# Kernel optimization log

Hardware: AMD Instinct MI355X
Metric: run time of the kernel (lower is better)

## Reference

```python
import jax, jax.numpy as jnp
import numpy as np

B, N, D = 4, 2048, 1024
H, A, Lv = 8, 128, 128   # heads, attention_dim (qk), linear_dim (v)
NUM_BLOCKS = 4
QKV_W = (2 * Lv + 2 * A) * H  # 4096
NEG = -1e9


def setup_inputs() -> dict:
    key = jax.random.key(0)
    ks = jax.random.split(key, 10)
    past_lengths = jax.random.randint(ks[0], (B,), 0, N)
    past_ids = jax.random.randint(ks[1], (B, N), 0, 10000)
    past_embeddings = jax.random.normal(ks[2], (B, N, D), dtype=jnp.float32)
    # per-block parameters, stacked on leading block axis (xavier-ish scale)
    qkv_w = jax.random.normal(ks[3], (NUM_BLOCKS, D, QKV_W), dtype=jnp.float32) * (1.0 / np.sqrt(D))
    qkv_b = jnp.zeros((NUM_BLOCKS, QKV_W), dtype=jnp.float32)
    out_w = jax.random.normal(ks[4], (NUM_BLOCKS, Lv * H, D), dtype=jnp.float32) * (1.0 / np.sqrt(Lv * H))
    out_b = jnp.zeros((NUM_BLOCKS, D), dtype=jnp.float32)
    ln_g = jnp.ones((NUM_BLOCKS, D), dtype=jnp.float32)
    ln_b = jnp.zeros((NUM_BLOCKS, D), dtype=jnp.float32)
    return {"past_lengths": past_lengths, "past_ids": past_ids,
            "past_embeddings": past_embeddings, "qkv_w": qkv_w, "qkv_b": qkv_b,
            "out_w": out_w, "out_b": out_b, "ln_g": ln_g, "ln_b": ln_b}


def _layer_norm(x, g, b, eps=1e-5):
    mu = jnp.mean(x, axis=-1, keepdims=True)
    var = jnp.mean(jnp.square(x - mu), axis=-1, keepdims=True)
    return (x - mu) * jax.lax.rsqrt(var + eps) * g + b


def _block(x, mask, qw, qb, ow, ob, g, b):
    xn = _layer_norm(x, g, b)
    qkv = (xn @ qw + qb).reshape(B, N, H, 2 * Lv + 2 * A)
    q = qkv[..., :A]              # [B,N,H,A]
    k = qkv[..., A:2 * A]         # [B,N,H,A]
    v = qkv[..., 2 * A:2 * A + Lv]  # [B,N,H,Lv]
    scores = jnp.einsum('bnha,bmha->bhnm', q, k) / np.sqrt(A)
    # original: masked_fill(-inf) -> silu -> /N -> softmax; we mask after the
    # silu transform with a large-negative logit so masked weights are ~0
    logits = jnp.where(mask[:, None, :, :], jax.nn.silu(scores) / N, NEG)
    w = jax.nn.softmax(logits, axis=-1)
    attn = jnp.einsum('bhnm,bmhl->bnhl', w, v).reshape(B, N, H * Lv)
    return x + attn @ ow + ob


def reference(past_lengths, past_ids, past_embeddings, qkv_w, qkv_b, out_w, out_b, ln_g, ln_b):
    valid = past_ids != 0                                   # [B,N]
    causal = jnp.triu(jnp.ones((N, N), dtype=bool), k=1)     # faithful to buffer (triu, diag=1)
    mask = causal[None] & valid[:, None, :] & valid[:, :, None]  # [B,N,N]
    x = past_embeddings
    for i in range(NUM_BLOCKS):
        x = _block(x, mask, qkv_w[i], qkv_b[i], out_w[i], out_b[i], ln_g[i], ln_b[i])
    return x
```

## Files before the change

kernel.cpp:

```cpp
#include <hip/hip_runtime.h>

typedef __bf16 bf16_t;
typedef __bf16 bf16x8 __attribute__((ext_vector_type(8)));
typedef __bf16 bf16x4 __attribute__((ext_vector_type(4)));
typedef float f32x4 __attribute__((ext_vector_type(4)));
typedef unsigned int u32x4 __attribute__((ext_vector_type(4)));

#define B_ 4
#define N_ 2048
#define D_ 1024
#define H_ 8
#define NB_ 4
#define M_ (B_*N_)
#define QN_ 3072
#define QKN_ 2048

__device__ __forceinline__ void async_copy16(const void* gsrc, void* ldst) {
    __builtin_amdgcn_global_load_lds(
        (const __attribute__((address_space(1))) void*)gsrc,
        (__attribute__((address_space(3))) void*)ldst, 16, 0, 0);
}

static constexpr size_t WT_OFF  = 0;
static constexpr size_t WT_SZ   = (size_t)NB_*QN_*D_*2;
static constexpr size_t OWT_OFF = WT_OFF + WT_SZ;
static constexpr size_t OWT_SZ  = (size_t)NB_*D_*D_*2;
static constexpr size_t XN_OFF  = OWT_OFF + OWT_SZ;
static constexpr size_t XN_SZ   = (size_t)M_*D_*2;
static constexpr size_t QK_OFF  = XN_OFF + XN_SZ;
static constexpr size_t QK_SZ   = (size_t)M_*QKN_*2;
static constexpr size_t VT_OFF  = QK_OFF + QK_SZ;
static constexpr size_t VT_SZ   = (size_t)32*128*N_*2;
static constexpr size_t ATT_OFF = VT_OFF + VT_SZ;
static constexpr size_t ATT_SZ  = (size_t)M_*D_*2;
static constexpr size_t QBR_OFF = ATT_OFF + ATT_SZ;
static constexpr size_t QBR_SZ  = (size_t)NB_*QN_*4;
static constexpr size_t VS_OFF  = QBR_OFF + QBR_SZ;
static constexpr size_t VS_SZ   = (size_t)NB_*32*128*4;
static constexpr size_t MASK_OFF = VS_OFF + VS_SZ;

__global__ __launch_bounds__(256) void repack_qkvw(const float* __restrict__ qw, bf16_t* __restrict__ wt)
{
    __shared__ float tile[64][65];
    const int nb = blockIdx.z;
    const int j0 = blockIdx.x * 64, d0 = blockIdx.y * 64;
    const int tx = threadIdx.x, ty = threadIdx.y;
    const float* src = qw + (size_t)nb * D_ * 4096;
    const int jj = j0 + tx;
    const int sel = jj >> 10, rr = jj & 1023, hh = rr >> 7, aa = rr & 127;
    const int orig = hh * 512 + sel * 128 + aa;
#pragma unroll
    for (int it = 0; it < 16; ++it) {
        int dr = it * 4 + ty;
        tile[dr][tx] = src[(size_t)(d0 + dr) * 4096 + orig];
    }
    __syncthreads();
    bf16_t* dst = wt + (size_t)nb * QN_ * D_;
#pragma unroll
    for (int it = 0; it < 16; ++it) {
        int jr = it * 4 + ty;
        dst[(size_t)(j0 + jr) * D_ + d0 + tx] = (bf16_t)tile[tx][jr];
    }
}

__global__ __launch_bounds__(256) void repack_outw(const float* __restrict__ ow, bf16_t* __restrict__ owt)
{
    __shared__ float tile[64][65];
    const int nb = blockIdx.z;
    const int j0 = blockIdx.x * 64, d0 = blockIdx.y * 64;
    const int tx = threadIdx.x, ty = threadIdx.y;
    const float* src = ow + (size_t)nb * D_ * D_;
#pragma unroll
    for (int it = 0; it < 16; ++it) {
        int dr = it * 4 + ty;
        tile[dr][tx] = src[(size_t)(d0 + dr) * D_ + j0 + tx];
    }
    __syncthreads();
    bf16_t* dst = owt + (size_t)nb * D_ * D_;
#pragma unroll
    for (int it = 0; it < 16; ++it) {
        int jr = it * 4 + ty;
        dst[(size_t)(j0 + jr) * D_ + d0 + tx] = (bf16_t)tile[tx][jr];
    }
}

__global__ __launch_bounds__(256) void repack_qb(const float* __restrict__ qb, float* __restrict__ qbr)
{
    int idx = blockIdx.x * 256 + threadIdx.x;
    int nb = idx / QN_, jj = idx % QN_;
    int sel = jj >> 10, rr = jj & 1023, hh = rr >> 7, aa = rr & 127;
    qbr[idx] = qb[nb * 4096 + hh * 512 + sel * 128 + aa];
}

__global__ __launch_bounds__(256) void mask_kernel(const int* __restrict__ past_ids, unsigned short* __restrict__ maskA,
                                                   float* __restrict__ vsl)
{
    const int idx = blockIdx.x * 256 + threadIdx.x;
    vsl[idx] = 0.f; vsl[idx + 8192] = 0.f;
    const int b = idx >> 11, P = idx & 2047;
    const int k = P & 31;
    const int m = (P & ~31) | (((k >> 2) & 1) << 4) | (((k >> 3) & 3) << 2) | (k & 3);
    maskA[idx] = past_ids[b * N_ + m] != 0 ? 0xFFFFu : 0u;
}

__global__ __launch_bounds__(256) void ln_kernel(const float* __restrict__ x, const float* __restrict__ g,
                                                 const float* __restrict__ bb, bf16_t* __restrict__ xn)
{
    const int row = blockIdx.x, tid = threadIdx.x;
    const float4 v = ((const float4*)(x + (size_t)row * D_))[tid];
    float s = v.x + v.y + v.z + v.w;
    float q = v.x * v.x + v.y * v.y + v.z * v.z + v.w * v.w;
#pragma unroll
    for (int d = 32; d >= 1; d >>= 1) { s += __shfl_xor(s, d); q += __shfl_xor(q, d); }
    __shared__ float ls[4], lq[4];
    if ((tid & 63) == 0) { ls[tid >> 6] = s; lq[tid >> 6] = q; }
    __syncthreads();
    s = ls[0] + ls[1] + ls[2] + ls[3];
    q = lq[0] + lq[1] + lq[2] + lq[3];
    const float mean = s * (1.f / 1024.f);
    const float var  = q * (1.f / 1024.f) - mean * mean;
    const float inv  = rsqrtf(var + 1e-5f);
    const float4 gg = ((const float4*)g)[tid];
    const float4 bv = ((const float4*)bb)[tid];
    bf16x4 o;
    o[0] = (bf16_t)((v.x - mean) * inv * gg.x + bv.x);
    o[1] = (bf16_t)((v.y - mean) * inv * gg.y + bv.y);
    o[2] = (bf16_t)((v.z - mean) * inv * gg.z + bv.z);
    o[3] = (bf16_t)((v.w - mean) * inv * gg.w + bv.w);
    *(bf16x4*)(xn + (size_t)row * D_ + tid * 4) = o;
}

__global__ __launch_bounds__(512, 2) void gemm_qkv(const bf16_t* __restrict__ Am, const bf16_t* __restrict__ Bt,
                                                   const float* __restrict__ bias,
                                                   bf16_t* __restrict__ outQK, bf16_t* __restrict__ vtOut,
                                                   float* __restrict__ vsOut)
{
    __shared__ bf16_t As[2 * 16384];
    __shared__ bf16_t Bs[2 * 12288];
    const int tid = threadIdx.x;
    const int lane = tid & 63, wave = tid >> 6;
    const int wr = wave >> 2, wc = wave & 3;
    const int quad = lane >> 4, l15 = lane & 15;
    const int swz = quad ^ ((l15 >> 1) & 3);
    const int slane8 = ((lane & 3) ^ ((lane >> 3) & 3)) * 8;
    const int lrow = lane >> 2;
    const int m0 = blockIdx.y * 256, n0 = blockIdx.x * 192;
    const int Kn = D_;

    const bf16_t* gA[4]; bf16_t* dA[4];
    const bf16_t* gB[3]; bf16_t* dB[3];
#pragma unroll
    for (int u = 0; u < 4; ++u) {
        const int a = wave * 4 + u, ch = a >> 1, hf = a & 1;
        gA[u] = Am + (size_t)(m0 + ch * 16 + lrow) * Kn + hf * 32 + slane8;
        dA[u] = &As[hf * 8192 + ch * 512 + lane * 8];
    }
#pragma unroll
    for (int u = 0; u < 3; ++u) {
        const int b = wave * 3 + u, ch = b >> 1, hf = b & 1;
        gB[u] = Bt + (size_t)(n0 + ch * 16 + lrow) * Kn + hf * 32 + slane8;
        dB[u] = &Bs[hf * 6144 + ch * 512 + lane * 8];
    }

    auto STAGE = [&](int slot) {
#pragma unroll
        for (int u = 0; u < 4; ++u) { async_copy16(gA[u], dA[u] + slot * 16384); gA[u] += 64; }
#pragma unroll
        for (int u = 0; u < 3; ++u) { async_copy16(gB[u], dB[u] + slot * 12288); gB[u] += 64; }
    };

    f32x4 acc[8][3] = {};
    const int NT = Kn >> 6;

    STAGE(0);
    asm volatile("s_waitcnt vmcnt(0)" ::: "memory");
    __builtin_amdgcn_s_barrier();

    const int abase = wr * 4096 + l15 * 32 + swz * 8;
    const int bbase = wc * 1536 + l15 * 32 + swz * 8;

    for (int t = 0; t < NT; ++t) {
        const int slot = t & 1;
        const bf16_t* ra = &As[slot * 16384 + abase];
        const bf16_t* rb = &Bs[slot * 12288 + bbase];
        if (t + 1 < NT) STAGE(slot ^ 1);
        __builtin_amdgcn_s_setprio(1);
#pragma unroll
        for (int hf = 0; hf < 2; ++hf) {
            bf16x8 af[8], bfv[3];
#pragma unroll
            for (int j = 0; j < 3; ++j) bfv[j] = *(const bf16x8*)(rb + hf * 6144 + j * 512);
#pragma unroll
            for (int i = 0; i < 8; ++i) af[i] = *(const bf16x8*)(ra + hf * 8192 + i * 512);
#pragma unroll
            for (int i = 0; i < 8; ++i)
#pragma unroll
                for (int j = 0; j < 3; ++j)
                    acc[i][j] = __builtin_amdgcn_mfma_f32_16x16x32_bf16(af[i], bfv[j], acc[i][j], 0, 0, 0);
        }
        __builtin_amdgcn_s_setprio(0);
        if (t + 1 < NT) asm volatile("s_waitcnt vmcnt(0)" ::: "memory");
        __builtin_amdgcn_s_barrier();
    }

    const int bb2 = m0 >> 11;
    int colgj[3]; float bvj[3];
#pragma unroll
    for (int j = 0; j < 3; ++j) { colgj[j] = n0 + wc * 48 + j * 16 + l15; bvj[j] = bias[colgj[j]]; }
    float ps[3] = {0.f, 0.f, 0.f};
#pragma unroll
    for (int i = 0; i < 8; ++i) {
        const int rowg = m0 + wr * 128 + i * 16 + quad * 4;
        const int mloc = rowg & 2047;
        const int mperm = (mloc & ~31) | (((mloc >> 2) & 3) << 3) | (((mloc >> 4) & 1) << 2);
#pragma unroll
        for (int j = 0; j < 3; ++j) {
            const int colg = colgj[j];
            const float bv = bvj[j];
            if (colg >= 2048) {
                const int hh = (colg - 2048) >> 7, ll = (colg - 2048) & 127;
                bf16x4 sv;
#pragma unroll
                for (int r = 0; r < 4; ++r) { sv[r] = (bf16_t)(acc[i][j][r] + bv); ps[j] += acc[i][j][r]; }
                *(bf16x4*)(vtOut + ((size_t)(bb2 * 8 + hh) * 128 + ll) * (size_t)N_ + mperm) = sv;
            } else {
                const float qs = (colg < 1024) ? 0.08838834764831845f : 1.f;
#pragma unroll
                for (int r = 0; r < 4; ++r)
                    outQK[(size_t)(rowg + r) * QKN_ + colg] = (bf16_t)((acc[i][j][r] + bv) * qs);
            }
        }
    }
#pragma unroll
    for (int j = 0; j < 3; ++j) {
        const int colg = colgj[j];
        if (colg >= 2048) {
            const int hh = (colg - 2048) >> 7, ll = (colg - 2048) & 127;
            float p = ps[j] + 32.f * bvj[j];
            p += __shfl_xor(p, 16);
            p += __shfl_xor(p, 32);
            if (quad == 0) atomicAdd(&vsOut[(size_t)(bb2 * 8 + hh) * 128 + ll], p);
        }
    }
}

__global__ __launch_bounds__(512, 2) void gemm_out(const bf16_t* __restrict__ Am, const bf16_t* __restrict__ Bt,
                                                   const float* __restrict__ bias,
                                                   const float* __restrict__ resid_in, float* __restrict__ resid_out)
{
    __shared__ bf16_t As[4 * 256 * 32];
    __shared__ bf16_t Bs[4 * 128 * 32];
    const int tid = threadIdx.x;
    const int lane = tid & 63, wave = tid >> 6;
    const int wr = wave >> 2, wc = wave & 3;
    const int quad = lane >> 4, l15 = lane & 15;
    const int swz = quad ^ ((l15 >> 1) & 3);
    const int slane8 = ((lane & 3) ^ ((lane >> 3) & 3)) * 8;
    const int lrow = lane >> 2;
    const int m0 = blockIdx.y * 256, n0 = blockIdx.x * 128;
    const int Kn = D_;

    const int chA0 = wave * 2, chA1 = chA0 + 1;
    const bf16_t* gA0 = Am + (size_t)(m0 + chA0 * 16 + lrow) * Kn + slane8;
    const bf16_t* gA1 = Am + (size_t)(m0 + chA1 * 16 + lrow) * Kn + slane8;
    const bf16_t* gB  = Bt + (size_t)(n0 + wave * 16 + lrow) * Kn + slane8;
    bf16_t* const dA0 = &As[chA0 * 512 + lane * 8];
    bf16_t* const dA1 = &As[chA1 * 512 + lane * 8];
    bf16_t* const dB  = &Bs[wave * 512 + lane * 8];

    auto STAGE = [&](int slot) {
        async_copy16(gA0, dA0 + slot * 8192);
        async_copy16(gA1, dA1 + slot * 8192);
        async_copy16(gB,  dB  + slot * 4096);
        gA0 += 32; gA1 += 32; gB += 32;
    };

    f32x4 acc[8][2] = {};
    const int NT = Kn >> 5;

    STAGE(0); STAGE(1); STAGE(2);
    asm volatile("s_waitcnt vmcnt(6)" ::: "memory");
    __builtin_amdgcn_s_barrier();

    const int aoff = (wr * 128 + l15) * 32 + swz * 8;
    const int boff = (wc * 32  + l15) * 32 + swz * 8;

    for (int t = 0; t < NT; ++t) {
        const int ring = t & 3;
        const bf16_t* ra = &As[ring * 8192 + aoff];
        const bf16_t* rb = &Bs[ring * 4096 + boff];
        bf16x8 af[8], bfv[2];
#pragma unroll
        for (int j = 0; j < 2; ++j) bfv[j] = *(const bf16x8*)(rb + j * 512);
#pragma unroll
        for (int i = 0; i < 8; ++i) af[i] = *(const bf16x8*)(ra + i * 512);
        if (t + 3 < NT) STAGE((t + 3) & 3);
        __builtin_amdgcn_s_setprio(1);
#pragma unroll
        for (int i = 0; i < 8; ++i)
#pragma unroll
            for (int j = 0; j < 2; ++j)
                acc[i][j] = __builtin_amdgcn_mfma_f32_16x16x32_bf16(af[i], bfv[j], acc[i][j], 0, 0, 0);
        __builtin_amdgcn_s_setprio(0);
        if (t + 3 < NT)      asm volatile("s_waitcnt vmcnt(6)" ::: "memory");
        else if (t + 2 < NT) asm volatile("s_waitcnt vmcnt(3)" ::: "memory");
        else if (t + 1 < NT) asm volatile("s_waitcnt vmcnt(0)" ::: "memory");
        __builtin_amdgcn_s_barrier();
    }

#pragma unroll
    for (int i = 0; i < 8; ++i) {
#pragma unroll
        for (int j = 0; j < 2; ++j) {
            const int colg = n0 + wc * 32 + j * 16 + l15;
            const float bv = bias[colg];
#pragma unroll
            for (int r = 0; r < 4; ++r) {
                const int rowg = m0 + wr * 128 + i * 16 + quad * 4 + r;
                const size_t off = (size_t)rowg * D_ + colg;
                resid_out[off] = resid_in[off] + acc[i][j][r] + bv;
            }
        }
    }
}

template<bool CAUSAL>
__device__ __forceinline__ void attn_tile(
    int m0, int m0n, int n0, int b, int h,
    const bf16_t* __restrict__ qk, const bf16_t* __restrict__ vtb,
    const unsigned short* __restrict__ maskB,
    bf16_t* Ks, bf16_t* Vs,
    const bf16x8 (&qf)[2][4], bf16x8 onesf,
    f32x4 (&oacc)[2][8], f32x4 (&dacc)[2])
{
    const int tid = threadIdx.x, lane = tid & 63, wave = tid >> 6;
    const int quad = lane >> 4, l15 = lane & 15;
    const int swz = quad ^ ((l15 >> 1) & 3);
    const int slane8 = ((lane & 3) ^ ((lane >> 3) & 3)) * 8;
    const int lrow = lane >> 2;
    const float invN = 1.f / 2048.f;

#pragma unroll
    for (int s = 0; s < 8; ++s) {
        const int kkc = s & 3, rg = (s >> 2) + wave * 2;
        async_copy16(vtb + (size_t)(rg * 16 + lrow) * N_ + m0 + kkc * 32 + slane8,
                     &Vs[kkc * 4096 + rg * 512 + lane * 8]);
    }
    bf16x8 mAf[4];
#pragma unroll
    for (int kk = 0; kk < 4; ++kk)
        mAf[kk] = *(const bf16x8*)(maskB + m0 + kk * 32 + quad * 8);

    f32x4 sacc[2][8] = {};
    __builtin_amdgcn_s_setprio(1);
#pragma unroll
    for (int kk = 0; kk < 4; ++kk) {
#pragma unroll
        for (int j = 0; j < 8; ++j) {
            bf16x8 kf = *(const bf16x8*)&Ks[kk * 4096 + (j * 16 + l15) * 32 + swz * 8];
            sacc[0][j] = __builtin_amdgcn_mfma_f32_16x16x32_bf16(kf, qf[0][kk], sacc[0][j], 0, 0, 0);
            sacc[1][j] = __builtin_amdgcn_mfma_f32_16x16x32_bf16(kf, qf[1][kk], sacc[1][j], 0, 0, 0);
        }
    }
    __builtin_amdgcn_s_setprio(0);

    bf16x8 pf[2][4];
#pragma unroll
    for (int kk = 0; kk < 4; ++kk) {
#pragma unroll
        for (int s = 0; s < 2; ++s) {
            const int j = kk * 2 + s;
#pragma unroll
            for (int nb = 0; nb < 2; ++nb) {
#pragma unroll
                for (int r = 0; r < 4; ++r) {
                    const float sv = sacc[nb][j][r];
                    const float xc = __builtin_amdgcn_fmed3f(sv, -4.f, 4.f);
                    float sg = __builtin_fmaf(xc, 0.25f * invN, 0.5f * invN);
                    sg = __builtin_fmaf(-(xc * (0.03125f * invN)), fabsf(xc), sg);
                    float e = __builtin_fmaf(sv, sg, 1.f);
                    if (CAUSAL) {
                        const int dmn = (m0 + j * 16 + quad * 4 + r) - (n0 + wave * 32 + nb * 16 + l15);
                        e = (dmn > 0) ? e : 0.f;
                    }
                    pf[nb][kk][s * 4 + r] = (bf16_t)e;
                }
            }
        }
        *(u32x4*)&pf[0][kk] = *(u32x4*)&pf[0][kk] & *(const u32x4*)&mAf[kk];
        *(u32x4*)&pf[1][kk] = *(u32x4*)&pf[1][kk] & *(const u32x4*)&mAf[kk];
    }

    __syncthreads();

    if (m0n < N_) {
        const size_t baseq = (size_t)b * N_ * QKN_;
#pragma unroll
        for (int s = 0; s < 8; ++s) {
            const int kkc = s & 3, rg = (s >> 2) + wave * 2;
            async_copy16(qk + baseq + (size_t)(m0n + rg * 16 + lrow) * QKN_ + 1024 + h * 128 + kkc * 32 + slane8,
                         &Ks[kkc * 4096 + rg * 512 + lane * 8]);
        }
    }

    __builtin_amdgcn_s_setprio(1);
#pragma unroll
    for (int kk = 0; kk < 4; ++kk) {
        dacc[0] = __builtin_amdgcn_mfma_f32_16x16x32_bf16(pf[0][kk], onesf, dacc[0], 0, 0, 0);
        dacc[1] = __builtin_amdgcn_mfma_f32_16x16x32_bf16(pf[1][kk], onesf, dacc[1], 0, 0, 0);
#pragma unroll
        for (int j = 0; j < 8; ++j) {
            bf16x8 vf = *(const bf16x8*)&Vs[kk * 4096 + (j * 16 + l15) * 32 + swz * 8];
            oacc[0][j] = __builtin_amdgcn_mfma_f32_16x16x32_bf16(pf[0][kk], vf, oacc[0][j], 0, 0, 0);
            oacc[1][j] = __builtin_amdgcn_mfma_f32_16x16x32_bf16(pf[1][kk], vf, oacc[1][j], 0, 0, 0);
        }
    }
    __builtin_amdgcn_s_setprio(0);
    __syncthreads();
}

__global__ __launch_bounds__(256, 2) void attn_kernel(const bf16_t* __restrict__ qk, const bf16_t* __restrict__ vt,
                                                      const int* __restrict__ past_ids, const float* __restrict__ vsum,
                                                      const unsigned short* __restrict__ maskA,
                                                      bf16_t* __restrict__ att)
{
    __shared__ bf16_t Ks[4 * 128 * 32];
    __shared__ bf16_t Vs[4 * 128 * 32];

    const int bx = blockIdx.x;
    const int bh = bx & 31, g = bx >> 5;
    const int t = (g < 8) ? g : 23 - g;
    const int b = bh >> 3, h = bh & 7;
    const int n0 = t << 7;
    const int tid = threadIdx.x, lane = tid & 63, wave = tid >> 6;
    const int quad = lane >> 4, l15 = lane & 15;
    const int slane8 = ((lane & 3) ^ ((lane >> 3) & 3)) * 8;
    const int lrow = lane >> 2;
    const bf16_t* vtb = vt + (size_t)bh * 128 * N_;
    const unsigned short* maskB = maskA + b * N_;
    const float invN = 1.f / 2048.f;

    bf16x8 qf[2][4];
#pragma unroll
    for (int nb = 0; nb < 2; ++nb) {
        const bf16_t* gq = qk + (size_t)b * N_ * QKN_ + (size_t)(n0 + wave * 32 + nb * 16 + l15) * QKN_ + h * 128 + quad * 8;
#pragma unroll
        for (int kk = 0; kk < 4; ++kk) qf[nb][kk] = *(const bf16x8*)(gq + kk * 32);
    }
    const float vnf0 = past_ids[b * N_ + n0 + wave * 32 + l15] != 0 ? 1.f : 0.f;
    const float vnf1 = past_ids[b * N_ + n0 + wave * 32 + 16 + l15] != 0 ? 1.f : 0.f;
    bf16x8 onesf;
#pragma unroll
    for (int i = 0; i < 8; ++i) onesf[i] = (bf16_t)1.f;

    {
        const size_t baseq = (size_t)b * N_ * QKN_;
#pragma unroll
        for (int s = 0; s < 8; ++s) {
            const int kkc = s & 3, rg = (s >> 2) + wave * 2;
            async_copy16(qk + baseq + (size_t)(n0 + rg * 16 + lrow) * QKN_ + 1024 + h * 128 + kkc * 32 + slane8,
                         &Ks[kkc * 4096 + rg * 512 + lane * 8]);
        }
    }
    __syncthreads();

    f32x4 oacc[2][8] = {};
    f32x4 dacc[2] = {};

    attn_tile<true>(n0, n0 + 128, n0, b, h, qk, vtb, maskB, Ks, Vs, qf, onesf, oacc, dacc);
    for (int m0 = n0 + 128; m0 < N_; m0 += 128)
        attn_tile<false>(m0, m0 + 128, n0, b, h, qk, vtb, maskB, Ks, Vs, qf, onesf, oacc, dacc);

    float vsr[8];
#pragma unroll
    for (int j = 0; j < 8; ++j) vsr[j] = vsum[bh * 128 + j * 16 + l15];
#pragma unroll
    for (int nb = 0; nb < 2; ++nb) {
        const float vn = nb ? vnf1 : vnf0;
#pragma unroll
        for (int r = 0; r < 4; ++r) {
            const float dn = dacc[nb][r];
            const bool uni = (vn == 0.f) || !(dn > 0.f);
            const float rc = uni ? 0.f : __builtin_amdgcn_rcpf(dn);
            const int gn = n0 + wave * 32 + nb * 16 + quad * 4 + r;
#pragma unroll
            for (int j = 0; j < 8; ++j) {
                const float ov = uni ? (vsr[j] * invN) : (oacc[nb][j][r] * rc);
                att[(size_t)(b * N_ + gn) * 1024 + h * 128 + j * 16 + l15] = (bf16_t)ov;
            }
        }
    }
}

extern "C" void kernel_launch(void* const* d_in, const int* in_sizes, int n_in,
                              void* d_out, int out_size, void* d_ws, size_t ws_size,
                              hipStream_t stream) {
    (void)in_sizes; (void)n_in; (void)out_size; (void)ws_size;
    const int*   past_ids = (const int*)d_in[1];
    const float* past_emb = (const float*)d_in[2];
    const float* qkv_w    = (const float*)d_in[3];
    const float* qkv_b    = (const float*)d_in[4];
    const float* out_w    = (const float*)d_in[5];
    const float* out_b    = (const float*)d_in[6];
    const float* ln_g     = (const float*)d_in[7];
    const float* ln_b     = (const float*)d_in[8];

    float* x = (float*)d_out;
    char* ws = (char*)d_ws;
    bf16_t* WT  = (bf16_t*)(ws + WT_OFF);
    bf16_t* OWT = (bf16_t*)(ws + OWT_OFF);
    bf16_t* XN  = (bf16_t*)(ws + XN_OFF);
    bf16_t* QK  = (bf16_t*)(ws + QK_OFF);
    bf16_t* VT  = (bf16_t*)(ws + VT_OFF);
    bf16_t* ATT = (bf16_t*)(ws + ATT_OFF);
    float*  QBR = (float*)(ws + QBR_OFF);
    float*  VSL = (float*)(ws + VS_OFF);
    unsigned short* MASKA = (unsigned short*)(ws + MASK_OFF);

    repack_qkvw<<<dim3(48, 16, NB_), dim3(64, 4), 0, stream>>>(qkv_w, WT);
    repack_outw<<<dim3(16, 16, NB_), dim3(64, 4), 0, stream>>>(out_w, OWT);
    repack_qb<<<48, 256, 0, stream>>>(qkv_b, QBR);
    mask_kernel<<<32, 256, 0, stream>>>(past_ids, MASKA, VSL);

    for (int layer = 0; layer < NB_; ++layer) {
        const float* xin = (layer == 0) ? past_emb : x;
        ln_kernel<<<M_, 256, 0, stream>>>(xin, ln_g + layer * D_, ln_b + layer * D_, XN);
        gemm_qkv<<<dim3(QN_ / 192, M_ / 256), 512, 0, stream>>>(
            XN, WT + (size_t)layer * QN_ * D_, QBR + layer * QN_, QK, VT, VSL + layer * 4096);
        attn_kernel<<<512, 256, 0, stream>>>(QK, VT, past_ids, VSL + layer * 4096, MASKA, ATT);
        gemm_out<<<dim3(D_ / 128, M_ / 256), 512, 0, stream>>>(
            ATT, OWT + (size_t)layer * D_ * D_, out_b + layer * D_, xin, x);
    }
}
```

Measured before the change: 835.5 us.

## Rework QKV GEMM with 32x32 MFMA, 384-wide tiles and triple-buffered K=32 stages

The QKV projection GEMM now uses 32x32x16 MFMA instructions in place of 16x16x32, and widens the N tile from 192 to 384 columns, which halves the grid along N. The K loop switches to 32-element stages with a three-slot LDS ring, so two loads stay in flight (vmcnt(5)). The epilogue is rewritten for the 32x32 accumulator layout, keeping the V-transpose permutation and the column-sum atomics. The intent is more reuse per LDS read, fewer MFMA issues and deeper load pipelining. In exchange, the grid has fewer blocks, register pressure rises, and there are more barriers per unit of K.

```diff
diff --git a/kernel.cpp b/kernel.cpp
--- a/kernel.cpp
+++ b/kernel.cpp
@@ -4,6 +4,7 @@
 typedef __bf16 bf16x8 __attribute__((ext_vector_type(8)));
 typedef __bf16 bf16x4 __attribute__((ext_vector_type(4)));
 typedef float f32x4 __attribute__((ext_vector_type(4)));
+typedef float f32x16 __attribute__((ext_vector_type(16)));
 typedef unsigned int u32x4 __attribute__((ext_vector_type(4)));
 
 #define B_ 4
@@ -135,111 +136,123 @@
                                                    bf16_t* __restrict__ outQK, bf16_t* __restrict__ vtOut,
                                                    float* __restrict__ vsOut)
 {
-    __shared__ bf16_t As[2 * 16384];
-    __shared__ bf16_t Bs[2 * 12288];
+    __shared__ bf16_t As[3 * 8192];
+    __shared__ bf16_t Bs[3 * 12288];
     const int tid = threadIdx.x;
     const int lane = tid & 63, wave = tid >> 6;
     const int wr = wave >> 2, wc = wave & 3;
-    const int quad = lane >> 4, l15 = lane & 15;
-    const int swz = quad ^ ((l15 >> 1) & 3);
+    const int hi = lane >> 5;
+    const int rowin = lane & 15, chsel = (lane >> 4) & 1;
+    const int rsw = (rowin >> 1) & 3;
     const int slane8 = ((lane & 3) ^ ((lane >> 3) & 3)) * 8;
     const int lrow = lane >> 2;
-    const int m0 = blockIdx.y * 256, n0 = blockIdx.x * 192;
+    const int m0 = blockIdx.y * 256, n0 = blockIdx.x * 384;
     const int Kn = D_;
 
-    const bf16_t* gA[4]; bf16_t* dA[4];
-    const bf16_t* gB[3]; bf16_t* dB[3];
-#pragma unroll
-    for (int u = 0; u < 4; ++u) {
-        const int a = wave * 4 + u, ch = a >> 1, hf = a & 1;
-        gA[u] = Am + (size_t)(m0 + ch * 16 + lrow) * Kn + hf * 32 + slane8;
-        dA[u] = &As[hf * 8192 + ch * 512 + lane * 8];
-    }
-#pragma unroll
-    for (int u = 0; u < 3; ++u) {
-        const int b = wave * 3 + u, ch = b >> 1, hf = b & 1;
-        gB[u] = Bt + (size_t)(n0 + ch * 16 + lrow) * Kn + hf * 32 + slane8;
-        dB[u] = &Bs[hf * 6144 + ch * 512 + lane * 8];
-    }
+    const bf16_t* gA0 = Am + (size_t)(m0 + (wave * 2 + 0) * 16 + lrow) * Kn + slane8;
+    const bf16_t* gA1 = Am + (size_t)(m0 + (wave * 2 + 1) * 16 + lrow) * Kn + slane8;
+    const bf16_t* gB0 = Bt + (size_t)(n0 + (wave * 3 + 0) * 16 + lrow) * Kn + slane8;
+    const bf16_t* gB1 = Bt + (size_t)(n0 + (wave * 3 + 1) * 16 + lrow) * Kn + slane8;
+    const bf16_t* gB2 = Bt + (size_t)(n0 + (wave * 3 + 2) * 16 + lrow) * Kn + slane8;
+    bf16_t* const dA0 = &As[(wave * 2 + 0) * 512 + lane * 8];
+    bf16_t* const dA1 = &As[(wave * 2 + 1) * 512 + lane * 8];
+    bf16_t* const dB0 = &Bs[(wave * 3 + 0) * 512 + lane * 8];
+    bf16_t* const dB1 = &Bs[(wave * 3 + 1) * 512 + lane * 8];
+    bf16_t* const dB2 = &Bs[(wave * 3 + 2) * 512 + lane * 8];
 
     auto STAGE = [&](int slot) {
-#pragma unroll
-        for (int u = 0; u < 4; ++u) { async_copy16(gA[u], dA[u] + slot * 16384); gA[u] += 64; }
-#pragma unroll
-        for (int u = 0; u < 3; ++u) { async_copy16(gB[u], dB[u] + slot * 12288); gB[u] += 64; }
+        async_copy16(gA0, dA0 + slot * 8192);
+        async_copy16(gA1, dA1 + slot * 8192);
+        async_copy16(gB0, dB0 + slot * 12288);
+        async_copy16(gB1, dB1 + slot * 12288);
+        async_copy16(gB2, dB2 + slot * 12288);
+        gA0 += 32; gA1 += 32; gB0 += 32; gB1 += 32; gB2 += 32;
     };
 
-    f32x4 acc[8][3] = {};
-    const int NT = Kn >> 6;
-
-    STAGE(0);
-    asm volatile("s_waitcnt vmcnt(0)" ::: "memory");
+    f32x16 acc[4][3] = {};
+    const int NT = Kn >> 5;
+
+    STAGE(0); STAGE(1);
+    asm volatile("s_waitcnt vmcnt(5)" ::: "memory");
     __builtin_amdgcn_s_barrier();
 
-    const int abase = wr * 4096 + l15 * 32 + swz * 8;
-    const int bbase = wc * 1536 + l15 * 32 + swz * 8;
+    const int aix = (wr * 8 + chsel) * 512 + rowin * 32;
+    const int bix = (wc * 6 + chsel) * 512 + rowin * 32;
+    const int kc0 = (hi ^ rsw) * 8;
+    const int kc1 = ((2 + hi) ^ rsw) * 8;
 
     for (int t = 0; t < NT; ++t) {
-        const int slot = t & 1;
-        const bf16_t* ra = &As[slot * 16384 + abase];
-        const bf16_t* rb = &Bs[slot * 12288 + bbase];
-        if (t + 1 < NT) STAGE(slot ^ 1);
+        const int slot = t % 3;
+        const bf16_t* ra = &As[slot * 8192 + aix];
+        const bf16_t* rb = &Bs[slot * 12288 + bix];
+        bf16x8 af[4], bfv[3];
+#pragma unroll
+        for (int jb = 0; jb < 3; ++jb) bfv[jb] = *(const bf16x8*)(rb + jb * 1024 + kc0);
+#pragma unroll
+        for (int ib = 0; ib < 4; ++ib) af[ib] = *(const bf16x8*)(ra + ib * 1024 + kc0);
+        if (t + 2 < NT) STAGE((t + 2) % 3);
         __builtin_amdgcn_s_setprio(1);
 #pragma unroll
-        for (int hf = 0; hf < 2; ++hf) {
-            bf16x8 af[8], bfv[3];
-#pragma unroll
-            for (int j = 0; j < 3; ++j) bfv[j] = *(const bf16x8*)(rb + hf * 6144 + j * 512);
-#pragma unroll
-            for (int i = 0; i < 8; ++i) af[i] = *(const bf16x8*)(ra + hf * 8192 + i * 512);
-#pragma unroll
-            for (int i = 0; i < 8; ++i)
-#pragma unroll
-                for (int j = 0; j < 3; ++j)
-                    acc[i][j] = __builtin_amdgcn_mfma_f32_16x16x32_bf16(af[i], bfv[j], acc[i][j], 0, 0, 0);
-        }
+        for (int ib = 0; ib < 4; ++ib)
+#pragma unroll
+            for (int jb = 0; jb < 3; ++jb)
+                acc[ib][jb] = __builtin_amdgcn_mfma_f32_32x32x16_bf16(af[ib], bfv[jb], acc[ib][jb], 0, 0, 0);
+#pragma unroll
+        for (int jb = 0; jb < 3; ++jb) bfv[jb] = *(const bf16x8*)(rb + jb * 1024 + kc1);
+#pragma unroll
+        for (int ib = 0; ib < 4; ++ib) af[ib] = *(const bf16x8*)(ra + ib * 1024 + kc1);
+#pragma unroll
+        for (int ib = 0; ib < 4; ++ib)
+#pragma unroll
+            for (int jb = 0; jb < 3; ++jb)
+                acc[ib][jb] = __builtin_amdgcn_mfma_f32_32x32x16_bf16(af[ib], bfv[jb], acc[ib][jb], 0, 0, 0);
         __builtin_amdgcn_s_setprio(0);
-        if (t + 1 < NT) asm volatile("s_waitcnt vmcnt(0)" ::: "memory");
+        if (t + 2 < NT)      asm volatile("s_waitcnt vmcnt(5)" ::: "memory");
+        else if (t + 1 < NT) asm volatile("s_waitcnt vmcnt(0)" ::: "memory");
         __builtin_amdgcn_s_barrier();
     }
 
     const int bb2 = m0 >> 11;
-    int colgj[3]; float bvj[3];
-#pragma unroll
-    for (int j = 0; j < 3; ++j) { colgj[j] = n0 + wc * 48 + j * 16 + l15; bvj[j] = bias[colgj[j]]; }
-    float ps[3] = {0.f, 0.f, 0.f};
-#pragma unroll
-    for (int i = 0; i < 8; ++i) {
-        const int rowg = m0 + wr * 128 + i * 16 + quad * 4;
-        const int mloc = rowg & 2047;
-        const int mperm = (mloc & ~31) | (((mloc >> 2) & 3) << 3) | (((mloc >> 4) & 1) << 2);
-#pragma unroll
-        for (int j = 0; j < 3; ++j) {
-            const int colg = colgj[j];
-            const float bv = bvj[j];
-            if (colg >= 2048) {
-                const int hh = (colg - 2048) >> 7, ll = (colg - 2048) & 127;
-                bf16x4 sv;
-#pragma unroll
-                for (int r = 0; r < 4; ++r) { sv[r] = (bf16_t)(acc[i][j][r] + bv); ps[j] += acc[i][j][r]; }
-                *(bf16x4*)(vtOut + ((size_t)(bb2 * 8 + hh) * 128 + ll) * (size_t)N_ + mperm) = sv;
-            } else {
-                const float qs = (colg < 1024) ? 0.08838834764831845f : 1.f;
-#pragma unroll
-                for (int r = 0; r < 4; ++r)
-                    outQK[(size_t)(rowg + r) * QKN_ + colg] = (bf16_t)((acc[i][j][r] + bv) * qs);
-            }
-        }
-    }
-#pragma unroll
-    for (int j = 0; j < 3; ++j) {
-        const int colg = colgj[j];
+    const int colB = lane & 31;
+#pragma unroll
+    for (int jb = 0; jb < 3; ++jb) {
+        const int colg = n0 + wc * 96 + jb * 32 + colB;
+        const float bv = bias[colg];
         if (colg >= 2048) {
             const int hh = (colg - 2048) >> 7, ll = (colg - 2048) & 127;
-            float p = ps[j] + 32.f * bvj[j];
-            p += __shfl_xor(p, 16);
+            bf16_t* vrow = vtOut + ((size_t)(bb2 * 8 + hh) * 128 + ll) * (size_t)N_;
+            float p = 64.f * bv;
+#pragma unroll
+            for (int ib = 0; ib < 4; ++ib) {
+                const int mbase = (m0 + wr * 128 + ib * 32) & 2047;
+#pragma unroll
+                for (int u = 0; u < 4; ++u) {
+                    const int mp = mbase + 8 * ((2 * u + hi) & 3) + 4 * (u >> 1);
+                    bf16x4 sv;
+#pragma unroll
+                    for (int v = 0; v < 4; ++v) {
+                        const float x = acc[ib][jb][4 * u + v];
+                        sv[v] = (bf16_t)(x + bv);
+                        p += x;
+                    }
+                    *(bf16x4*)(vrow + mp) = sv;
+                }
+            }
             p += __shfl_xor(p, 32);
-            if (quad == 0) atomicAdd(&vsOut[(size_t)(bb2 * 8 + hh) * 128 + ll], p);
+            if (hi == 0) atomicAdd(&vsOut[(size_t)(bb2 * 8 + hh) * 128 + ll], p);
+        } else {
+            const float qs = (colg < 1024) ? 0.08838834764831845f : 1.f;
+#pragma unroll
+            for (int ib = 0; ib < 4; ++ib) {
+                const int rbase = m0 + wr * 128 + ib * 32 + 4 * hi;
+#pragma unroll
+                for (int u = 0; u < 4; ++u)
+#pragma unroll
+                    for (int v = 0; v < 4; ++v) {
+                        const int m = rbase + 8 * u + v;
+                        outQK[(size_t)m * QKN_ + colg] = (bf16_t)((acc[ib][jb][4 * u + v] + bv) * qs);
+                    }
+            }
         }
     }
 }
@@ -525,7 +538,7 @@
     for (int layer = 0; layer < NB_; ++layer) {
         const float* xin = (layer == 0) ? past_emb : x;
         ln_kernel<<<M_, 256, 0, stream>>>(xin, ln_g + layer * D_, ln_b + layer * D_, XN);
-        gemm_qkv<<<dim3(QN_ / 192, M_ / 256), 512, 0, stream>>>(
+        gemm_qkv<<<dim3(QN_ / 384, M_ / 256), 512, 0, stream>>>(
             XN, WT + (size_t)layer * QN_ * D_, QBR + layer * QN_, QK, VT, VSL + layer * 4096);
         attn_kernel<<<512, 256, 0, stream>>>(QK, VT, past_ids, VSL + layer * 4096, MASKA, ATT);
         gemm_out<<<dim3(D_ / 128, M_ / 256), 512, 0, stream>>>(
```

Measured after the change: 827.4 us. About the same (-1.0%).
